# Kernel optimization log

Hardware: AMD Instinct MI355X
Metric: run time of the kernel (lower is better)

The kernel has to match this reference:

```python
import jax, jax.numpy as jnp
import numpy as np

N, E = 50000, 800000
IN, HID, PROJ = 256, 256, 256


def setup_inputs() -> dict:
    key = jax.random.key(0)
    ks = jax.random.split(key, 6)
    x = jax.random.normal(ks[0], (N, IN), dtype=jnp.float32)
    edge_index = jax.random.randint(ks[1], (2, E), 0, N, dtype=jnp.int32)
    # GCNConv params: Linear (no bias inside lin; bias added after aggregation)
    W1 = jax.random.normal(ks[2], (IN, HID), dtype=jnp.float32) / np.sqrt(IN)
    b1 = jnp.zeros((HID,), dtype=jnp.float32)
    W2 = jax.random.normal(ks[3], (HID, PROJ), dtype=jnp.float32) / np.sqrt(HID)
    b2 = jnp.zeros((PROJ,), dtype=jnp.float32)
    # shared PReLU parameter (PyTorch default init 0.25, single shared scalar)
    a = jnp.asarray(0.25, dtype=jnp.float32)
    return {"x": x, "W1": W1, "b1": b1, "W2": W2, "b2": b2, "a": a,
            "edge_index": edge_index}


def _prelu(x, a):
    return jnp.where(x >= 0, x, a * x)


def _gcn_conv(x, W, b, src, dst, norm):
    # GCNConv: out = D^-1/2 (A + I) D^-1/2 (x W) + b
    h = x @ W                                      # [N, out]
    msg = h[src] * norm[:, None]                   # [E+N, out] edge messages
    out = jax.ops.segment_sum(msg, dst, num_segments=N)
    return out + b


def reference(x, W1, b1, W2, b2, a, edge_index):
    src, dst = edge_index[0], edge_index[1]
    loop = jnp.arange(N, dtype=src.dtype)
    src = jnp.concatenate([src, loop])             # add self-loops
    dst = jnp.concatenate([dst, loop])
    # symmetric normalization (degree counted on dst, as in PyG gcn_norm)
    deg = jax.ops.segment_sum(jnp.ones_like(dst, jnp.float32), dst,
                              num_segments=N)
    dinv = jax.lax.rsqrt(jnp.maximum(deg, 1.0))    # deg >= 1 with self-loops
    norm = dinv[src] * dinv[dst]                   # [E+N]
    h = _prelu(_gcn_conv(x, W1, b1, src, dst, norm), a)
    h = _prelu(_gcn_conv(h, W2, b2, src, dst, norm), a)
    return h
```

## Files before the change

kernel.cpp:

```cpp
#include <hip/hip_runtime.h>

#define NN 50000
#define EE 800000
#define FF 256
#define NBLK 196
#define GEMM_BLKS 784
#define FILL_BLKS 1563
#define CNT_BLKS  3125
#define G1_BLKS   2352

typedef float    f32x4 __attribute__((ext_vector_type(4)));
typedef _Float16 f16x8 __attribute__((ext_vector_type(8)));
typedef _Float16 f16x4 __attribute__((ext_vector_type(4)));


__global__ __launch_bounds__(256) void scan_part(const int* __restrict__ ec,
                                                 int* __restrict__ bsum) {
    int i = blockIdx.x * 256 + threadIdx.x;
    int v = (i < NN) ? ec[i] : 0;
#pragma unroll
    for (int d = 1; d < 64; d <<= 1) v += __shfl_xor(v, d);
    __shared__ int wt[4];
    int lane = threadIdx.x & 63, wid = threadIdx.x >> 6;
    if (lane == 0) wt[wid] = v;
    __syncthreads();
    if (threadIdx.x == 0)
        bsum[blockIdx.x] = wt[0] + wt[1] + wt[2] + wt[3];
}

__global__ __launch_bounds__(256) void scan_final(const int* __restrict__ ec,
                                                  const int* __restrict__ bsum,
                                                  int* __restrict__ rs,
                                                  float* __restrict__ dinv) {
    const int t    = threadIdx.x;
    const int lane = t & 63, wid = t >> 6;
    __shared__ int wt[4];
    __shared__ int adds;

    int pv = (t < blockIdx.x && t < NBLK) ? bsum[t] : 0;
#pragma unroll
    for (int d = 1; d < 64; d <<= 1) pv += __shfl_xor(pv, d);
    if (lane == 0) wt[wid] = pv;
    __syncthreads();
    if (t == 0) adds = wt[0] + wt[1] + wt[2] + wt[3];
    __syncthreads();
    const int badd = adds;

    int i = blockIdx.x * 256 + t;
    int v = (i < NN) ? ec[i] : 0;
    int x = v;
#pragma unroll
    for (int d = 1; d < 64; d <<= 1) {
        int u = __shfl_up(x, d);
        if (lane >= d) x += u;
    }
    __syncthreads();
    if (lane == 63) wt[wid] = x;
    __syncthreads();
    int add = badd;
    for (int wi = 0; wi < wid; ++wi) add += wt[wi];
    x += add;
    if (i < NN) {
        rs[i]   = x - v;
        dinv[i] = rsqrtf((float)(v + 1));
    }
    if (i == 0) rs[NN] = EE;
}

__global__ void packw_kernel(const float* __restrict__ W1, const float* __restrict__ W2,
                             _Float16* __restrict__ wp,
                             const int* __restrict__ ei, int* __restrict__ ec) {
    if (blockIdx.x >= 64) {
        int e = (blockIdx.x - 64) * 256 + threadIdx.x;
        atomicAdd(&ec[ei[EE + e]], 1);
        return;
    }
    int idx = blockIdx.x * 256 + threadIdx.x;
    int p   = idx & 511;
    int kt  = (idx >> 9) & 7;
    int nb  = (idx >> 12) & 1;
    int L   = (idx >> 13) & 1;
    const float* W = L ? W2 : W1;
    int rs = p >> 2, cs = p & 3;
    int r  = rs ^ ((rs >> 2) & 1);
    int c  = cs ^ (r & 3);
    int n  = nb * 128 + r;
    int k0 = kt * 32 + c * 8;
    f16x8 hi, lo;
#pragma unroll
    for (int j = 0; j < 8; ++j) {
        float v = W[(size_t)(k0 + j) * 256 + n];
        _Float16 h = (_Float16)v;
        hi[j] = h;
        lo[j] = (_Float16)(v - (float)h);
    }
    size_t ch = ((size_t)((L * 2 + 0) * 2 + nb) * 8 + kt) * 4096;
    size_t cl = ((size_t)((L * 2 + 1) * 2 + nb) * 8 + kt) * 4096;
    *(f16x8*)(wp + ch + (size_t)p * 8) = hi;
    *(f16x8*)(wp + cl + (size_t)p * 8) = lo;
}


__device__ __forceinline__ void gll16(const void* g, void* l) {
    __builtin_amdgcn_global_load_lds(
        (const __attribute__((address_space(1))) void*)g,
        (__attribute__((address_space(3))) void*)l, 16, 0, 0);
}

template<typename AT>
__global__ __launch_bounds__(512) void gemm_kernel(
    const AT* __restrict__ X, const _Float16* __restrict__ Bhi,
    const _Float16* __restrict__ Blo, _Float16* __restrict__ H,
    const int* __restrict__ ei, const int* __restrict__ rs,
    int* __restrict__ cnt, const float* __restrict__ dinv,
    int2* __restrict__ ecw) {
    __shared__ __align__(16) _Float16 Bh[2][4096];
    __shared__ __align__(16) _Float16 Bl[2][4096];
    __shared__ __align__(16) AT       As[2][4096];

    int gid;
    if constexpr (sizeof(AT) == 4) {
        const int bid = blockIdx.x;
        if (bid % 3 != 0) {
            int fill_id = bid - bid / 3 - 1;
            if (fill_id < FILL_BLKS) {
                int e = fill_id * 512 + threadIdx.x;
                if (e < EE) {
                    int s = ei[e];
                    int d = ei[EE + e];
                    int p = rs[d] + atomicAdd(&cnt[d], 1);
                    ecw[p] = make_int2(s, __float_as_int(dinv[s]));
                }
            }
            return;
        }
        gid = bid / 3;
    } else {
        gid = blockIdx.x;
    }

    const int p_  = (gid >> 4) * 8 + (gid & 7);
    const int nb  = (gid >> 3) & 1;
    if (p_ >= 391) return;

    const int tid = threadIdx.x;
    const int ln  = tid & 63;
    const int w   = tid >> 6;
    const int wm  = w & 1;
    const int wn  = w >> 1;
    const int q   = ln >> 4;
    const int l16 = ln & 15;
    const int m0  = p_ * 128;
    const size_t bchunk = (size_t)nb * 8 * 4096;

    f32x4 acc[4][2] = {};

    auto stage = [&](int kt, int buf) {
        int g = w * 64 + ln;
        gll16(Bhi + bchunk + (size_t)kt * 4096 + (size_t)g * 8,
              &Bh[buf][w * 512]);
        gll16(Blo + bchunk + (size_t)kt * 4096 + (size_t)g * 8,
              &Bl[buf][w * 512]);
        if constexpr (sizeof(AT) == 4) {
#pragma unroll
            for (int pp = 0; pp < 2; ++pp) {
                int gg = pp * 512 + w * 64 + ln;
                int rss = gg >> 3, cs = gg & 7;
                int c  = cs ^ (rss & 7);
                int gm = m0 + rss; if (gm > NN - 1) gm = NN - 1;
                gll16((const float*)X + (size_t)gm * FF + kt * 32 + c * 4,
                      (float*)&As[buf][0] + (size_t)(pp * 512 + w * 64) * 4);
            }
        } else {
            int rss = g >> 2, cs = g & 3;
            int r  = rss ^ ((rss >> 2) & 1);
            int c  = cs ^ (r & 3);
            int gm = m0 + r; if (gm > NN - 1) gm = NN - 1;
            gll16((const _Float16*)X + (size_t)gm * FF + kt * 32 + c * 8,
                  (_Float16*)&As[buf][0] + (size_t)(w * 64) * 8);
        }
    };

    auto compute = [&](int buf) {
        f16x8 af[4], bhf[2], blf[2];
#pragma unroll
        for (int mt = 0; mt < 4; ++mt) {
            int r = wm * 64 + mt * 16 + l16;
            if constexpr (sizeof(AT) == 4) {
                const float* Ab = (const float*)&As[buf][0];
                f32x4 v0 = *(const f32x4*)(Ab + (size_t)(r * 8 + ((2 * q)     ^ (r & 7))) * 4);
                f32x4 v1 = *(const f32x4*)(Ab + (size_t)(r * 8 + ((2 * q + 1) ^ (r & 7))) * 4);
                f16x8 a;
                a[0] = (_Float16)v0.x; a[1] = (_Float16)v0.y;
                a[2] = (_Float16)v0.z; a[3] = (_Float16)v0.w;
                a[4] = (_Float16)v1.x; a[5] = (_Float16)v1.y;
                a[6] = (_Float16)v1.z; a[7] = (_Float16)v1.w;
                af[mt] = a;
            } else {
                const _Float16* Ab = (const _Float16*)&As[buf][0];
                int rr = r ^ ((r >> 2) & 1);
                af[mt] = *(const f16x8*)(Ab + (size_t)(rr * 4 + (q ^ (r & 3))) * 8);
            }
        }
#pragma unroll
        for (int nt = 0; nt < 2; ++nt) {
            int r  = wn * 32 + nt * 16 + l16;
            int rr = r ^ ((r >> 2) & 1);
            int off = (rr * 4 + (q ^ (r & 3))) * 8;
            bhf[nt] = *(const f16x8*)(&Bh[buf][off]);
            blf[nt] = *(const f16x8*)(&Bl[buf][off]);
        }
#pragma unroll
        for (int mt = 0; mt < 4; ++mt)
#pragma unroll
            for (int nt = 0; nt < 2; ++nt) {
                acc[mt][nt] = __builtin_amdgcn_mfma_f32_16x16x32_f16(af[mt], bhf[nt], acc[mt][nt], 0, 0, 0);
                acc[mt][nt] = __builtin_amdgcn_mfma_f32_16x16x32_f16(af[mt], blf[nt], acc[mt][nt], 0, 0, 0);
            }
    };

    stage(0, 0);
    __syncthreads();
    int cur = 0;
#pragma unroll
    for (int kt = 0; kt < 8; ++kt) {
        if (kt < 7) stage(kt + 1, cur ^ 1);
        compute(cur);
        __syncthreads();
        cur ^= 1;
    }

#pragma unroll
    for (int mt = 0; mt < 4; ++mt)
#pragma unroll
        for (int r4 = 0; r4 < 4; ++r4) {
            int m = m0 + wm * 64 + mt * 16 + q * 4 + r4;
            if (m < NN) {
#pragma unroll
                for (int nt = 0; nt < 2; ++nt) {
                    int n = nb * 128 + wn * 32 + nt * 16 + l16;
                    H[(size_t)m * FF + n] = (_Float16)acc[mt][nt][r4];
                }
            }
        }
}

template<typename OT>
__global__ __launch_bounds__(256) void agg_kernel(
    const _Float16* __restrict__ H, const int* __restrict__ rs,
    const int2* __restrict__ ecw, const float* __restrict__ dinv,
    const float* __restrict__ bias, const float* __restrict__ a_ptr,
    OT* __restrict__ out) {
    const int row  = blockIdx.x * 4 + (threadIdx.x >> 6);
    const int lane = threadIdx.x & 63;
    if (row >= NN) return;

    const float av = a_ptr[0];
    const float di = dinv[row];

    f16x4 hv = *(const f16x4*)(H + (size_t)row * FF + lane * 4);
    float ax = di * (float)hv.x;
    float ay = di * (float)hv.y;
    float az = di * (float)hv.z;
    float aw = di * (float)hv.w;

    int e   = rs[row];
    int end = rs[row + 1];
    for (; e + 7 < end; e += 8) {
        int2 p0 = ecw[e],     p1 = ecw[e + 1], p2 = ecw[e + 2], p3 = ecw[e + 3];
        int2 p4 = ecw[e + 4], p5 = ecw[e + 5], p6 = ecw[e + 6], p7 = ecw[e + 7];
        f16x4 h0 = *(const f16x4*)(H + (size_t)p0.x * FF + lane * 4);
        f16x4 h1 = *(const f16x4*)(H + (size_t)p1.x * FF + lane * 4);
        f16x4 h2 = *(const f16x4*)(H + (size_t)p2.x * FF + lane * 4);
        f16x4 h3 = *(const f16x4*)(H + (size_t)p3.x * FF + lane * 4);
        f16x4 h4 = *(const f16x4*)(H + (size_t)p4.x * FF + lane * 4);
        f16x4 h5 = *(const f16x4*)(H + (size_t)p5.x * FF + lane * 4);
        f16x4 h6 = *(const f16x4*)(H + (size_t)p6.x * FF + lane * 4);
        f16x4 h7 = *(const f16x4*)(H + (size_t)p7.x * FF + lane * 4);
        float w0 = __int_as_float(p0.y), w1 = __int_as_float(p1.y);
        float w2 = __int_as_float(p2.y), w3 = __int_as_float(p3.y);
        float w4 = __int_as_float(p4.y), w5 = __int_as_float(p5.y);
        float w6 = __int_as_float(p6.y), w7 = __int_as_float(p7.y);
        ax += w0 * (float)h0.x + w1 * (float)h1.x + w2 * (float)h2.x + w3 * (float)h3.x
            + w4 * (float)h4.x + w5 * (float)h5.x + w6 * (float)h6.x + w7 * (float)h7.x;
        ay += w0 * (float)h0.y + w1 * (float)h1.y + w2 * (float)h2.y + w3 * (float)h3.y
            + w4 * (float)h4.y + w5 * (float)h5.y + w6 * (float)h6.y + w7 * (float)h7.y;
        az += w0 * (float)h0.z + w1 * (float)h1.z + w2 * (float)h2.z + w3 * (float)h3.z
            + w4 * (float)h4.z + w5 * (float)h5.z + w6 * (float)h6.z + w7 * (float)h7.z;
        aw += w0 * (float)h0.w + w1 * (float)h1.w + w2 * (float)h2.w + w3 * (float)h3.w
            + w4 * (float)h4.w + w5 * (float)h5.w + w6 * (float)h6.w + w7 * (float)h7.w;
    }
    for (; e + 3 < end; e += 4) {
        int2 p0 = ecw[e], p1 = ecw[e + 1], p2 = ecw[e + 2], p3 = ecw[e + 3];
        f16x4 h0 = *(const f16x4*)(H + (size_t)p0.x * FF + lane * 4);
        f16x4 h1 = *(const f16x4*)(H + (size_t)p1.x * FF + lane * 4);
        f16x4 h2 = *(const f16x4*)(H + (size_t)p2.x * FF + lane * 4);
        f16x4 h3 = *(const f16x4*)(H + (size_t)p3.x * FF + lane * 4);
        float w0 = __int_as_float(p0.y), w1 = __int_as_float(p1.y);
        float w2 = __int_as_float(p2.y), w3 = __int_as_float(p3.y);
        ax += w0 * (float)h0.x + w1 * (float)h1.x + w2 * (float)h2.x + w3 * (float)h3.x;
        ay += w0 * (float)h0.y + w1 * (float)h1.y + w2 * (float)h2.y + w3 * (float)h3.y;
        az += w0 * (float)h0.z + w1 * (float)h1.z + w2 * (float)h2.z + w3 * (float)h3.z;
        aw += w0 * (float)h0.w + w1 * (float)h1.w + w2 * (float)h2.w + w3 * (float)h3.w;
    }
    for (; e < end; ++e) {
        int2 p = ecw[e];
        float w0 = __int_as_float(p.y);
        f16x4 h0 = *(const f16x4*)(H + (size_t)p.x * FF + lane * 4);
        ax += w0 * (float)h0.x;
        ay += w0 * (float)h0.y;
        az += w0 * (float)h0.z;
        aw += w0 * (float)h0.w;
    }

    f32x4 bv = *(const f32x4*)(bias + lane * 4);
    float r0 = di * ax + bv.x; r0 = (r0 >= 0.f) ? r0 : av * r0;
    float r1 = di * ay + bv.y; r1 = (r1 >= 0.f) ? r1 : av * r1;
    float r2 = di * az + bv.z; r2 = (r2 >= 0.f) ? r2 : av * r2;
    float r3 = di * aw + bv.w; r3 = (r3 >= 0.f) ? r3 : av * r3;
    if constexpr (sizeof(OT) == 4) {
        f32x4 res = {r0, r1, r2, r3};
        *(f32x4*)((float*)out + (size_t)row * FF + lane * 4) = res;
    } else {
        f16x4 res;
        res.x = (_Float16)r0; res.y = (_Float16)r1;
        res.z = (_Float16)r2; res.w = (_Float16)r3;
        *(f16x4*)((_Float16*)out + (size_t)row * FF + lane * 4) = res;
    }
}

extern "C" void kernel_launch(void* const* d_in, const int* in_sizes, int n_in,
                              void* d_out, int out_size, void* d_ws, size_t ws_size,
                              hipStream_t stream) {
    const float* x  = (const float*)d_in[0];
    const float* W1 = (const float*)d_in[1];
    const float* b1 = (const float*)d_in[2];
    const float* W2 = (const float*)d_in[3];
    const float* b2 = (const float*)d_in[4];
    const float* a  = (const float*)d_in[5];
    const int*   ei = (const int*)d_in[6];
    float* out = (float*)d_out;

    char* ws = (char*)d_ws;
    size_t off = 0;
    auto carve = [&](size_t bytes) -> char* {
        char* p = ws + off;
        off = (off + bytes + 255) & ~(size_t)255;
        return p;
    };
    int*      ec   = (int*)carve((size_t)NN * 4);
    int*      cnt  = (int*)carve((size_t)NN * 4);
    int*      rs   = (int*)carve((size_t)(NN + 1) * 4);
    float*    dinv = (float*)carve((size_t)NN * 4);
    int*      bsum = (int*)carve((size_t)NBLK * 4);
    int2*     ecw  = (int2*)carve((size_t)EE * 8);
    _Float16* wp   = (_Float16*)carve((size_t)4 * 65536 * 2);
    _Float16* h    = (_Float16*)carve((size_t)NN * FF * 2);
    _Float16* h1   = (_Float16*)carve((size_t)NN * FF * 2);

    hipMemsetAsync(ec, 0, (size_t)NN * 4, stream);
    hipMemsetAsync(cnt, 0, (size_t)NN * 4, stream);

    packw_kernel<<<64 + CNT_BLKS, 256, 0, stream>>>(W1, W2, wp, ei, ec);

    scan_part <<<NBLK, 256, 0, stream>>>(ec, bsum);
    scan_final<<<NBLK, 256, 0, stream>>>(ec, bsum, rs, dinv);

    gemm_kernel<float><<<G1_BLKS, 512, 0, stream>>>(
        x, wp, wp + 65536, h, ei, rs, cnt, dinv, ecw);

    agg_kernel<_Float16><<<(NN + 3) / 4, 256, 0, stream>>>(h, rs, ecw, dinv, b1, a, h1);
    gemm_kernel<_Float16><<<GEMM_BLKS, 512, 0, stream>>>(
        h1, wp + 131072, wp + 131072 + 65536, h, nullptr, nullptr, nullptr, nullptr, nullptr);
    agg_kernel<float><<<(NN + 3) / 4, 256, 0, stream>>>(h, rs, ecw, dinv, b2, a, out);
}
```

Measured before the change: 343.5 us.

## Convert fp32 A tile to fp16 at staging and reorder fused fill blocks

The first-layer GEMM now loads fp32 X rows into registers, converts them to fp16 once, and writes them to shared memory in the same swizzled fp16 layout used by the second GEMM. This replaces the async fp32 LDS staging and the per-compute conversion, halving the LDS footprint and removing repeated conversions across warps. The CSR fill blocks are moved after all GEMM blocks instead of being interleaved, and the cnt memset is folded into scan_final. The register-staged loads lose the async global-to-LDS path and may expose load latency, which is only partly hidden behind compute.

```diff
diff --git a/kernel.cpp b/kernel.cpp
--- a/kernel.cpp
+++ b/kernel.cpp
@@ -7,7 +7,6 @@
 #define GEMM_BLKS 784
 #define FILL_BLKS 1563
 #define CNT_BLKS  3125
-#define G1_BLKS   2352
 
 typedef float    f32x4 __attribute__((ext_vector_type(4)));
 typedef _Float16 f16x8 __attribute__((ext_vector_type(8)));
@@ -31,7 +30,8 @@
 __global__ __launch_bounds__(256) void scan_final(const int* __restrict__ ec,
                                                   const int* __restrict__ bsum,
                                                   int* __restrict__ rs,
-                                                  float* __restrict__ dinv) {
+                                                  float* __restrict__ dinv,
+                                                  int* __restrict__ cnt) {
     const int t    = threadIdx.x;
     const int lane = t & 63, wid = t >> 6;
     __shared__ int wt[4];
@@ -63,6 +63,7 @@
     if (i < NN) {
         rs[i]   = x - v;
         dinv[i] = rsqrtf((float)(v + 1));
+        cnt[i]  = 0;
     }
     if (i == 0) rs[NN] = EE;
 }
@@ -116,29 +117,22 @@
     int2* __restrict__ ecw) {
     __shared__ __align__(16) _Float16 Bh[2][4096];
     __shared__ __align__(16) _Float16 Bl[2][4096];
-    __shared__ __align__(16) AT       As[2][4096];
-
-    int gid;
+    __shared__ __align__(16) _Float16 As[2][4096];
+
     if constexpr (sizeof(AT) == 4) {
-        const int bid = blockIdx.x;
-        if (bid % 3 != 0) {
-            int fill_id = bid - bid / 3 - 1;
-            if (fill_id < FILL_BLKS) {
-                int e = fill_id * 512 + threadIdx.x;
-                if (e < EE) {
-                    int s = ei[e];
-                    int d = ei[EE + e];
-                    int p = rs[d] + atomicAdd(&cnt[d], 1);
-                    ecw[p] = make_int2(s, __float_as_int(dinv[s]));
-                }
+        if (blockIdx.x >= GEMM_BLKS) {
+            int e = (blockIdx.x - GEMM_BLKS) * 512 + threadIdx.x;
+            if (e < EE) {
+                int s = ei[e];
+                int d = ei[EE + e];
+                int p = rs[d] + atomicAdd(&cnt[d], 1);
+                ecw[p] = make_int2(s, __float_as_int(dinv[s]));
             }
             return;
         }
-        gid = bid / 3;
-    } else {
-        gid = blockIdx.x;
-    }
-
+    }
+
+    const int gid = blockIdx.x;
     const int p_  = (gid >> 4) * 8 + (gid & 7);
     const int nb  = (gid >> 3) & 1;
     if (p_ >= 391) return;
@@ -153,54 +147,45 @@
     const int m0  = p_ * 128;
     const size_t bchunk = (size_t)nb * 8 * 4096;
 
+    const int g   = w * 64 + ln;
+    const int rs_ = g >> 2, cs_ = g & 3;
+    const int r_  = rs_ ^ ((rs_ >> 2) & 1);
+    const int c_  = cs_ ^ (r_ & 3);
+    int gm_ = m0 + r_; if (gm_ > NN - 1) gm_ = NN - 1;
+
     f32x4 acc[4][2] = {};
 
-    auto stage = [&](int kt, int buf) {
-        int g = w * 64 + ln;
+    auto stageB = [&](int kt, int buf) {
         gll16(Bhi + bchunk + (size_t)kt * 4096 + (size_t)g * 8,
               &Bh[buf][w * 512]);
         gll16(Blo + bchunk + (size_t)kt * 4096 + (size_t)g * 8,
               &Bl[buf][w * 512]);
-        if constexpr (sizeof(AT) == 4) {
-#pragma unroll
-            for (int pp = 0; pp < 2; ++pp) {
-                int gg = pp * 512 + w * 64 + ln;
-                int rss = gg >> 3, cs = gg & 7;
-                int c  = cs ^ (rss & 7);
-                int gm = m0 + rss; if (gm > NN - 1) gm = NN - 1;
-                gll16((const float*)X + (size_t)gm * FF + kt * 32 + c * 4,
-                      (float*)&As[buf][0] + (size_t)(pp * 512 + w * 64) * 4);
-            }
-        } else {
-            int rss = g >> 2, cs = g & 3;
-            int r  = rss ^ ((rss >> 2) & 1);
-            int c  = cs ^ (r & 3);
-            int gm = m0 + r; if (gm > NN - 1) gm = NN - 1;
-            gll16((const _Float16*)X + (size_t)gm * FF + kt * 32 + c * 8,
-                  (_Float16*)&As[buf][0] + (size_t)(w * 64) * 8);
-        }
+    };
+    auto stageA16 = [&](int kt, int buf) {
+        gll16((const _Float16*)X + (size_t)gm_ * FF + kt * 32 + c_ * 8,
+              (_Float16*)&As[buf][0] + (size_t)(w * 64) * 8);
+    };
+    auto loadA32 = [&](int kt, f32x4& v0, f32x4& v1) {
+        const float* p = (const float*)X + (size_t)gm_ * FF + kt * 32 + c_ * 8;
+        v0 = *(const f32x4*)p;
+        v1 = *(const f32x4*)(p + 4);
+    };
+    auto writeA32 = [&](int buf, f32x4 v0, f32x4 v1) {
+        f16x8 a;
+        a[0] = (_Float16)v0.x; a[1] = (_Float16)v0.y;
+        a[2] = (_Float16)v0.z; a[3] = (_Float16)v0.w;
+        a[4] = (_Float16)v1.x; a[5] = (_Float16)v1.y;
+        a[6] = (_Float16)v1.z; a[7] = (_Float16)v1.w;
+        *(f16x8*)(&As[buf][(size_t)g * 8]) = a;
     };
 
     auto compute = [&](int buf) {
         f16x8 af[4], bhf[2], blf[2];
 #pragma unroll
         for (int mt = 0; mt < 4; ++mt) {
-            int r = wm * 64 + mt * 16 + l16;
-            if constexpr (sizeof(AT) == 4) {
-                const float* Ab = (const float*)&As[buf][0];
-                f32x4 v0 = *(const f32x4*)(Ab + (size_t)(r * 8 + ((2 * q)     ^ (r & 7))) * 4);
-                f32x4 v1 = *(const f32x4*)(Ab + (size_t)(r * 8 + ((2 * q + 1) ^ (r & 7))) * 4);
-                f16x8 a;
-                a[0] = (_Float16)v0.x; a[1] = (_Float16)v0.y;
-                a[2] = (_Float16)v0.z; a[3] = (_Float16)v0.w;
-                a[4] = (_Float16)v1.x; a[5] = (_Float16)v1.y;
-                a[6] = (_Float16)v1.z; a[7] = (_Float16)v1.w;
-                af[mt] = a;
-            } else {
-                const _Float16* Ab = (const _Float16*)&As[buf][0];
-                int rr = r ^ ((r >> 2) & 1);
-                af[mt] = *(const f16x8*)(Ab + (size_t)(rr * 4 + (q ^ (r & 3))) * 8);
-            }
+            int r  = wm * 64 + mt * 16 + l16;
+            int rr = r ^ ((r >> 2) & 1);
+            af[mt] = *(const f16x8*)(&As[buf][(rr * 4 + (q ^ (r & 3))) * 8]);
         }
 #pragma unroll
         for (int nt = 0; nt < 2; ++nt) {
@@ -219,15 +204,36 @@
             }
     };
 
-    stage(0, 0);
-    __syncthreads();
     int cur = 0;
-#pragma unroll
-    for (int kt = 0; kt < 8; ++kt) {
-        if (kt < 7) stage(kt + 1, cur ^ 1);
-        compute(cur);
+    if constexpr (sizeof(AT) == 4) {
+        f32x4 v0, v1;
+        loadA32(0, v0, v1);
+        stageB(0, 0);
+        writeA32(0, v0, v1);
         __syncthreads();
-        cur ^= 1;
+#pragma unroll
+        for (int kt = 0; kt < 8; ++kt) {
+            f32x4 n0, n1;
+            if (kt < 7) {
+                loadA32(kt + 1, n0, n1);
+                stageB(kt + 1, cur ^ 1);
+            }
+            compute(cur);
+            if (kt < 7) writeA32(cur ^ 1, n0, n1);
+            __syncthreads();
+            cur ^= 1;
+        }
+    } else {
+        stageA16(0, 0);
+        stageB(0, 0);
+        __syncthreads();
+#pragma unroll
+        for (int kt = 0; kt < 8; ++kt) {
+            if (kt < 7) { stageA16(kt + 1, cur ^ 1); stageB(kt + 1, cur ^ 1); }
+            compute(cur);
+            __syncthreads();
+            cur ^= 1;
+        }
     }
 
 #pragma unroll
@@ -359,14 +365,13 @@
     _Float16* h1   = (_Float16*)carve((size_t)NN * FF * 2);
 
     hipMemsetAsync(ec, 0, (size_t)NN * 4, stream);
-    hipMemsetAsync(cnt, 0, (size_t)NN * 4, stream);
 
     packw_kernel<<<64 + CNT_BLKS, 256, 0, stream>>>(W1, W2, wp, ei, ec);
 
     scan_part <<<NBLK, 256, 0, stream>>>(ec, bsum);
-    scan_final<<<NBLK, 256, 0, stream>>>(ec, bsum, rs, dinv);
-
-    gemm_kernel<float><<<G1_BLKS, 512, 0, stream>>>(
+    scan_final<<<NBLK, 256, 0, stream>>>(ec, bsum, rs, dinv, cnt);
+
+    gemm_kernel<float><<<GEMM_BLKS + FILL_BLKS, 512, 0, stream>>>(
         x, wp, wp + 65536, h, ei, rs, cnt, dinv, ecw);
 
     agg_kernel<_Float16><<<(NN + 3) / 4, 256, 0, stream>>>(h, rs, ecw, dinv, b1, a, h1);
```

Measured after the change: 340.2 us. No clear change (-1.0%).
